# Kernel tuning notes

Measured on AMD Instinct MI355X. Metric: run time of the kernel, lower is better.

## Reference

```python
import jax, jax.numpy as jnp
import numpy as np

EPS = 1e-12
K_APPNP = 3
ALPHA = 0.5

def setup_inputs() -> dict:
    key = jax.random.key(0)
    kg, kz, k1, k2, k3 = jax.random.split(key, 5)
    N, out_dim, hid_dim = 10000, 128, 256
    g = jax.random.uniform(kg, (N, N), dtype=jnp.float32)
    z = jax.random.normal(kz, (N, out_dim), dtype=jnp.float32)
    def xavier(k, shape):
        fan_out, fan_in = shape
        lim = float(np.sqrt(6.0 / (fan_in + fan_out)))
        return jax.random.uniform(k, shape, jnp.float32, -lim, lim)
    # torch Linear weight is [out_features, in_features]
    W1 = xavier(k1, (hid_dim, out_dim))    # res1: out_dim -> hid_dim
    W1_ = xavier(k2, (hid_dim, hid_dim))   # res1_: hid -> hid
    W2 = xavier(k3, (out_dim, hid_dim))    # res2: hid -> out_dim
    return {"g": g, "z": z, "W1": W1, "W1_": W1_, "W2": W2}

def _graph_conv(g, x, W, act):
    # dropout is identity in eval mode
    return act((g @ x) @ W.T)

def _appnp(g, H):
    Z = H
    for _ in range(K_APPNP):
        Z = (1.0 - ALPHA) * (g @ Z) + ALPHA * H
    return Z

def reference(g, z, W1, W1_, W2):
    z1 = _graph_conv(g, z, W1, jax.nn.relu)       # [N, hid]
    z_ = _graph_conv(g, z1, W1_, jax.nn.relu)     # [N, hid]
    # torch.tensor(z_) detaches from the autograd graph
    zn = jax.lax.stop_gradient(z_)
    norm = jnp.maximum(jnp.linalg.norm(zn, axis=1, keepdims=True), EPS)
    zn = zn / norm                                 # F.normalize(p=2, dim=1)
    Z = _appnp(g, zn)                              # [N, hid]
    res = _graph_conv(g, z_, W2, jax.nn.sigmoid)   # [N, out]
    return (res, Z)
```

## Files before the change

### kernel.cpp

```cpp
#include <hip/hip_runtime.h>
#include <stdint.h>

typedef __attribute__((ext_vector_type(8))) short short8;
typedef __attribute__((ext_vector_type(4))) float f32x4;
typedef __attribute__((ext_vector_type(4))) unsigned short us4;

#define MFMA16(a,b,c) __builtin_amdgcn_mfma_f32_16x16x32_bf16((a),(b),(c),0,0,0)

static __device__ __forceinline__ float bf2f(unsigned short u){
  union { float f; unsigned int i; } c; c.i = ((unsigned int)u) << 16; return c.f;
}
static __device__ __forceinline__ unsigned short f2bf(float f){
  union { float f; unsigned int i; } c; c.f = f;
  unsigned int x = c.i;
  unsigned int r = x + 0x7fffu + ((x >> 16) & 1u);
  return (unsigned short)(r >> 16);
}
static __device__ __forceinline__ short8 pack8(const float* v){
  short8 r;
  #pragma unroll
  for (int i = 0; i < 8; ++i) r[i] = (short)f2bf(v[i]);
  return r;
}

typedef const __attribute__((address_space(1))) void cg_void;
typedef __attribute__((address_space(3))) void lds_void;
static __device__ __forceinline__ void gl_lds16(const void* g, void* l){
  __builtin_amdgcn_global_load_lds((cg_void*)g, (lds_void*)l, 16, 0, 0);
}

#define MROWS 10240LL
#define LDA   10048

__global__ void k_zero(unsigned short* __restrict__ g16, unsigned short* __restrict__ Tbuf){
  const long long i0 = (long long)blockIdx.x*256 + threadIdx.x;
  const long long NG = 192LL*LDA/8;
  short8 z = {0,0,0,0,0,0,0,0};
  for (long long c = i0; c < NG; c += (long long)gridDim.x*256)
    *(short8*)(g16 + 10048LL*LDA + c*8) = z;
  for (long long c = i0; c < 512*6; c += (long long)gridDim.x*256){
    int row = (int)(c/6), k = (int)(c%6);
    *(short8*)(Tbuf + (long long)row*LDA + 10000 + k*8) = z;
  }
}

__global__ void k_conv_w(const float* __restrict__ a, unsigned short* __restrict__ oa, int na4,
                         const float* __restrict__ b, unsigned short* __restrict__ ob, int nb4,
                         const float* __restrict__ c, unsigned short* __restrict__ oc, int nc4){
  for (int i = blockIdx.x*blockDim.x + threadIdx.x; i < na4 + nb4 + nc4;
       i += gridDim.x*blockDim.x){
    const float* src; unsigned short* dst; int j = i;
    if (j < na4){ src = a; dst = oa; }
    else if (j < na4 + nb4){ j -= na4; src = b; dst = ob; }
    else { j -= na4 + nb4; src = c; dst = oc; }
    float4 f = *(const float4*)(src + (long long)j*4);
    us4 v; v.x=f2bf(f.x); v.y=f2bf(f.y); v.z=f2bf(f.z); v.w=f2bf(f.w);
    *(us4*)(dst + (long long)j*4) = v;
  }
}

__global__ void k_tconv_z(const float* __restrict__ z, unsigned short* __restrict__ o){
  __shared__ unsigned short t[64][65];
  const int rb = blockIdx.x*64, cb = blockIdx.y*64;
  #pragma unroll
  for (int it = 0; it < 4; ++it){
    int idx = it*256 + threadIdx.x;
    int r = idx >> 4, c4 = (idx & 15) * 4;
    float4 f = {0.f,0.f,0.f,0.f};
    if (rb + r < 10000) f = *(const float4*)(z + (long long)(rb+r)*128 + cb + c4);
    t[c4+0][r] = f2bf(f.x); t[c4+1][r] = f2bf(f.y);
    t[c4+2][r] = f2bf(f.z); t[c4+3][r] = f2bf(f.w);
  }
  __syncthreads();
  #pragma unroll
  for (int it = 0; it < 4; ++it){
    int idx = it*256 + threadIdx.x;
    int ro = idx >> 4, co4 = (idx & 15) * 4;
    us4 v; v.x=t[ro][co4]; v.y=t[ro][co4+1]; v.z=t[ro][co4+2]; v.w=t[ro][co4+3];
    *(us4*)(o + (long long)(cb+ro)*LDA + rb + co4) = v;
  }
}

__global__ __launch_bounds__(256)
void k_gemm_t0(const float* __restrict__ g, const unsigned short* __restrict__ zT,
               unsigned short* __restrict__ g16, unsigned short* __restrict__ P, int S)
{
  constexpr int ldp = 128;
  __shared__ unsigned short sm[2][(64+128)*64];
  const int tid = threadIdx.x, w = tid >> 6, l = tid & 63;
  const int lr = l & 15, lk = l >> 4;
  const int wm = w >> 1, wn = w & 1;
  const int mBase = blockIdx.x * 64;
  const int s = blockIdx.z;
  const int kt0 = (157*s)/S, kt1 = (157*(s+1))/S;

  int arow[2], acol8[2];
  #pragma unroll
  for (int i = 0; i < 2; ++i){
    int ch = tid + 256*i;
    int row = ch >> 3, gr = ch & 7;
    arow[i] = row; acol8[i] = (gr ^ (row & 7)) * 8;
  }
  float fA[2][8];
  auto loadA = [&](int kt){
    #pragma unroll
    for (int i = 0; i < 2; ++i){
      int grow = mBase + arow[i];
      int col = kt*64 + acol8[i];
      if (grow < 10000 && col < 10000){
        float4 x = *(const float4*)(g + (long long)grow*10000 + col);
        float4 y = *(const float4*)(g + (long long)grow*10000 + col + 4);
        fA[i][0]=x.x; fA[i][1]=x.y; fA[i][2]=x.z; fA[i][3]=x.w;
        fA[i][4]=y.x; fA[i][5]=y.y; fA[i][6]=y.z; fA[i][7]=y.w;
      } else {
        #pragma unroll
        for (int j = 0; j < 8; ++j) fA[i][j] = 0.f;
      }
    }
  };
  auto writeA = [&](int buf, int kt){
    #pragma unroll
    for (int i = 0; i < 2; ++i){
      int ch = tid + 256*i;
      short8 v = pack8(fA[i]);
      *(short8*)(&sm[buf][ch*8]) = v;
      *(short8*)(g16 + (long long)(mBase + arow[i])*LDA + kt*64 + acol8[i]) = v;
    }
  };
  auto stageB = [&](int buf, int kt){
    unsigned short* dst = &sm[buf][64*64];
    const unsigned short* Bk = zT + (long long)kt*64;
    #pragma unroll
    for (int i = 0; i < 4; ++i){
      int c = i*256 + tid; int row = c >> 3, gr = c & 7;
      gl_lds16(Bk + (long long)row*LDA + ((gr ^ (row & 7))*8), dst + c*8);
    }
  };

  f32x4 acc[2][4];
  #pragma unroll
  for (int i = 0; i < 2; ++i)
    #pragma unroll
    for (int j = 0; j < 4; ++j){ f32x4 zz = {0.f,0.f,0.f,0.f}; acc[i][j] = zz; }

  loadA(kt0); stageB(0, kt0); writeA(0, kt0);
  int cur = 0;
  for (int kt = kt0; kt < kt1; ++kt){
    __syncthreads();
    const bool pf = (kt + 1 < kt1);
    if (pf){ loadA(kt+1); stageB(cur^1, kt+1); }
    const unsigned short* sp = &sm[cur][0];
    #pragma unroll
    for (int ks = 0; ks < 2; ++ks){
      short8 a[2], b[4];
      #pragma unroll
      for (int i = 0; i < 2; ++i){
        int row = wm*32 + i*16 + lr;
        a[i] = *(const short8*)(sp + row*64 + (((4*ks+lk) ^ (row & 7))*8));
      }
      #pragma unroll
      for (int j = 0; j < 4; ++j){
        int rb = wn*64 + j*16 + lr;
        b[j] = *(const short8*)(sp + 64*64 + rb*64 + (((4*ks+lk) ^ (rb & 7))*8));
      }
      #pragma unroll
      for (int i = 0; i < 2; ++i)
        #pragma unroll
        for (int j = 0; j < 4; ++j)
          acc[i][j] = MFMA16(a[i], b[j], acc[i][j]);
    }
    if (pf) writeA(cur^1, kt+1);
    cur ^= 1;
  }

  unsigned short* Pp = P + (long long)s*MROWS*ldp;
  #pragma unroll
  for (int i = 0; i < 2; ++i){
    const int row0 = mBase + wm*32 + i*16 + lk*4;
    #pragma unroll
    for (int j = 0; j < 4; ++j){
      const int col = wn*64 + j*16 + lr;
      #pragma unroll
      for (int r = 0; r < 4; ++r)
        Pp[(long long)(row0+r)*ldp + col] = f2bf(acc[i][j][r]);
    }
  }
}

__global__ __launch_bounds__(512)
void k_gemm8(const unsigned short* __restrict__ A,
             const unsigned short* __restrict__ B,
             unsigned short* __restrict__ P, int S, int ldp)
{
  __shared__ unsigned short sm[2][32768];

  const int tid = threadIdx.x;
  const int wid = tid >> 6, l = tid & 63;
  const int wm = wid >> 2, wn = wid & 3;
  const int lr = l & 15, lk = l >> 4;
  const int mBase = blockIdx.x * 256;
  const int nBase = blockIdx.y * 256;
  const int s = blockIdx.z;
  const int kt0 = (157*s)/S, kt1 = (157*(s+1))/S;

  const unsigned short* gsrc[8];
  int ldst[8];
  #pragma unroll
  for (int h = 0; h < 4; ++h){
    const unsigned short* base = (h < 2) ? A : B;
    const int rowBase = ((h < 2) ? mBase : nBase) + (h & 1) * 128;
    const int ldsOff = ((h < 2) ? 0 : 16384) + (h & 1) * 8192;
    #pragma unroll
    for (int i = 0; i < 2; ++i){
      int ch = tid + 512*i;
      int row = ch >> 3, gc = (ch & 7) ^ (row & 7);
      gsrc[h*2+i] = base + (long long)(rowBase + row)*LDA + gc*8;
      ldst[h*2+i] = ldsOff + ch*8;
    }
  }
  auto stage_tile = [&](unsigned short* dst, int kt){
    const long long ko = (long long)kt * 64;
    #pragma unroll
    for (int i = 0; i < 8; ++i)
      gl_lds16(gsrc[i] + ko, dst + ldst[i]);
  };

  f32x4 acc[8][4];
  #pragma unroll
  for (int i = 0; i < 8; ++i)
    #pragma unroll
    for (int j = 0; j < 4; ++j){ f32x4 zz = {0.f,0.f,0.f,0.f}; acc[i][j] = zz; }

  stage_tile(&sm[0][0], kt0);

  int cur = 0;
  for (int kt = kt0; kt < kt1; ++kt){
    const bool pf = (kt + 1 < kt1);
    unsigned short* nb = &sm[cur ^ 1][0];
    const unsigned short* sp = &sm[cur][0];

    if (pf){
      stage_tile(nb, kt + 1);
      __builtin_amdgcn_sched_barrier(0);
      asm volatile("s_waitcnt vmcnt(8)" ::: "memory");
    } else {
      asm volatile("s_waitcnt vmcnt(0)" ::: "memory");
    }
    __builtin_amdgcn_sched_barrier(0);
    __builtin_amdgcn_s_barrier();
    __builtin_amdgcn_sched_barrier(0);

    short8 bfr[4][2];
    #pragma unroll
    for (int jj = 0; jj < 4; ++jj){
      const int row = wn*64 + jj*16 + lr;
      #pragma unroll
      for (int ks = 0; ks < 2; ++ks)
        bfr[jj][ks] = *(const short8*)(sp + 16384 + row*64 + (((ks*4+lk) ^ (row & 7))*8));
    }
    #pragma unroll
    for (int ih = 0; ih < 2; ++ih){
      short8 af[4][2];
      #pragma unroll
      for (int ii = 0; ii < 4; ++ii){
        const int row = wm*128 + ih*64 + ii*16 + lr;
        #pragma unroll
        for (int ks = 0; ks < 2; ++ks)
          af[ii][ks] = *(const short8*)(sp + row*64 + (((ks*4+lk) ^ (row & 7))*8));
      }
      __builtin_amdgcn_s_setprio(1);
      #pragma unroll
      for (int ks = 0; ks < 2; ++ks)
        #pragma unroll
        for (int ii = 0; ii < 4; ++ii)
          #pragma unroll
          for (int jj = 0; jj < 4; ++jj)
            acc[ih*4+ii][jj] = MFMA16(af[ii][ks], bfr[jj][ks], acc[ih*4+ii][jj]);
      __builtin_amdgcn_s_setprio(0);
    }
    __builtin_amdgcn_sched_barrier(0);
    __builtin_amdgcn_s_barrier();
    __builtin_amdgcn_sched_barrier(0);
    cur ^= 1;
  }

  unsigned short* Pp = P + (long long)s*MROWS*ldp;
  #pragma unroll
  for (int i = 0; i < 8; ++i){
    const int row0 = mBase + wm*128 + i*16 + lk*4;
    #pragma unroll
    for (int j = 0; j < 4; ++j){
      const int col = nBase + wn*64 + j*16 + lr;
      #pragma unroll
      for (int r = 0; r < 4; ++r)
        Pp[(long long)(row0+r)*ldp + col] = f2bf(acc[i][j][r]);
    }
  }
}

template<int NW, int KW, int LDP, int S, int MODE>
__global__ __launch_bounds__(320)
void k_small(const unsigned short* __restrict__ P,
             const unsigned short* __restrict__ W,
             unsigned short* __restrict__ o1,
             unsigned short* __restrict__ o2,
             unsigned short* __restrict__ o3,
             float* __restrict__ of)
{
  const int tid = threadIdx.x, w = tid >> 6, l = tid & 63;
  const int lr = l & 15, lk = l >> 4;
  const int mBase = blockIdx.x * 80;
  constexpr int NF = NW/16;
  constexpr long long SSTR = MROWS*(long long)LDP;

  f32x4 acc[NF];
  #pragma unroll
  for (int f = 0; f < NF; ++f){ f32x4 zz = {0.f,0.f,0.f,0.f}; acc[f] = zz; }

  const unsigned short* ap = P + (long long)(mBase + 16*w + lr)*LDP + lk*8;
  #pragma unroll
  for (int kc = 0; kc < KW/32; ++kc){
    float av[8];
    short8 v0 = *(const short8*)(ap + kc*32);
    #pragma unroll
    for (int e = 0; e < 8; ++e) av[e] = bf2f((unsigned short)v0[e]);
    #pragma unroll
    for (int s2 = 1; s2 < S; ++s2){
      short8 v = *(const short8*)(ap + (long long)s2*SSTR + kc*32);
      #pragma unroll
      for (int e = 0; e < 8; ++e) av[e] += bf2f((unsigned short)v[e]);
    }
    short8 a = pack8(av);
    #pragma unroll
    for (int f = 0; f < NF; ++f){
      short8 b = *(const short8*)(W + (long long)(16*f+lr)*KW + kc*32 + lk*8);
      acc[f] = MFMA16(a, b, acc[f]);
    }
  }

  const int row0 = mBase + 16*w + lk*4;
  if constexpr (MODE == 2){
    #pragma unroll
    for (int f = 0; f < NF; ++f){
      const int col = 16*f + lr;
      #pragma unroll
      for (int r = 0; r < 4; ++r)
        of[(long long)(row0+r)*NW + col] = 1.0f / (1.0f + expf(-acc[f][r]));
    }
  } else if constexpr (MODE == 0){
    #pragma unroll
    for (int f = 0; f < NF; ++f){
      us4 v;
      #pragma unroll
      for (int r = 0; r < 4; ++r) v[r] = f2bf(fmaxf(acc[f][r], 0.0f));
      *(us4*)(o1 + (long long)(16*f+lr)*LDA + row0) = v;
    }
  } else {
    float ss[4] = {0.f,0.f,0.f,0.f};
    #pragma unroll
    for (int f = 0; f < NF; ++f)
      #pragma unroll
      for (int r = 0; r < 4; ++r){
        float v = fmaxf(acc[f][r], 0.0f);
        acc[f][r] = v;
        ss[r] += v*v;
      }
    #pragma unroll
    for (int r = 0; r < 4; ++r){
      #pragma unroll
      for (int off = 1; off <= 8; off <<= 1)
        ss[r] += __shfl_xor(ss[r], off, 64);
      ss[r] = 1.0f / fmaxf(sqrtf(ss[r]), 1e-12f);
    }
    #pragma unroll
    for (int f = 0; f < NF; ++f){
      const int col = 16*f + lr;
      us4 vz, vn;
      #pragma unroll
      for (int r = 0; r < 4; ++r){
        vz[r] = f2bf(acc[f][r]);
        vn[r] = f2bf(acc[f][r]*ss[r]);
        o3[(long long)(row0+r)*256 + col] = vn[r];
      }
      *(us4*)(o1 + (long long)col*LDA + row0) = vz;
      *(us4*)(o2 + (long long)col*LDA + row0) = vn;
    }
  }
}

__global__ void k_reduce_T(const unsigned short* __restrict__ P, int S, int ldp, int colOff,
                           unsigned short* __restrict__ outT,
                           const unsigned short* __restrict__ H)
{
  __shared__ unsigned short t[64][65];
  const int rb = blockIdx.x*64, cb = blockIdx.y*64;
  const long long stride = MROWS * (long long)ldp;
  #pragma unroll
  for (int it = 0; it < 4; ++it){
    int idx = it*256 + threadIdx.x;
    int r = idx >> 4, c4 = (idx & 15)*4;
    int row = rb + r;
    float sv[4] = {0.f,0.f,0.f,0.f};
    if (row < 10000){
      const unsigned short* p = P + (long long)row*ldp + colOff + cb + c4;
      for (int s2 = 0; s2 < S; ++s2){
        us4 tt = *(const us4*)(p + (long long)s2*stride);
        sv[0] += bf2f(tt.x); sv[1] += bf2f(tt.y);
        sv[2] += bf2f(tt.z); sv[3] += bf2f(tt.w);
      }
      us4 h = *(const us4*)(H + (long long)row*256 + cb + c4);
      sv[0] = 0.5f*sv[0] + 0.5f*bf2f(h.x);
      sv[1] = 0.5f*sv[1] + 0.5f*bf2f(h.y);
      sv[2] = 0.5f*sv[2] + 0.5f*bf2f(h.z);
      sv[3] = 0.5f*sv[3] + 0.5f*bf2f(h.w);
    }
    t[c4+0][r] = f2bf(sv[0]); t[c4+1][r] = f2bf(sv[1]);
    t[c4+2][r] = f2bf(sv[2]); t[c4+3][r] = f2bf(sv[3]);
  }
  __syncthreads();
  #pragma unroll
  for (int it = 0; it < 4; ++it){
    int idx = it*256 + threadIdx.x;
    int ro = idx >> 4, co4 = (idx & 15)*4;
    us4 v; v.x=t[ro][co4]; v.y=t[ro][co4+1]; v.z=t[ro][co4+2]; v.w=t[ro][co4+3];
    *(us4*)(outT + (long long)(cb+ro)*LDA + rb + co4) = v;
  }
}

__global__ void k_reduce2(const unsigned short* __restrict__ P, int S, int ldp,
                          float* __restrict__ out, const unsigned short* __restrict__ H)
{
  const long long stride = MROWS * (long long)ldp;
  const int idx = blockIdx.x*256 + threadIdx.x;
  const int row = idx >> 6;
  const int c4 = (idx & 63)*4;
  const unsigned short* p = P + (long long)row*ldp + c4;
  float sv[4] = {0.f,0.f,0.f,0.f};
  for (int s2 = 0; s2 < S; ++s2){
    us4 tt = *(const us4*)(p + (long long)s2*stride);
    sv[0] += bf2f(tt.x); sv[1] += bf2f(tt.y);
    sv[2] += bf2f(tt.z); sv[3] += bf2f(tt.w);
  }
  us4 h = *(const us4*)(H + (long long)row*256 + c4);
  float4 o;
  o.x = 0.5f*sv[0] + 0.5f*bf2f(h.x);
  o.y = 0.5f*sv[1] + 0.5f*bf2f(h.y);
  o.z = 0.5f*sv[2] + 0.5f*bf2f(h.z);
  o.w = 0.5f*sv[3] + 0.5f*bf2f(h.w);
  *(float4*)(out + (long long)row*256 + c4) = o;
}

extern "C" void kernel_launch(void* const* d_in, const int* in_sizes, int n_in,
                              void* d_out, int out_size, void* d_ws, size_t ws_size,
                              hipStream_t stream)
{
  const float* g   = (const float*)d_in[0];
  const float* z   = (const float*)d_in[1];
  const float* W1  = (const float*)d_in[2];
  const float* W1_ = (const float*)d_in[3];
  const float* W2  = (const float*)d_in[4];

  char* ws = (char*)d_ws;
  size_t off = 0;
  auto alloc = [&](size_t bytes)->void*{
    void* p = ws + off; off += (bytes + 255) & ~(size_t)255; return p;
  };
  unsigned short* g16  = (unsigned short*)alloc(10240ULL*10048*2);
  unsigned short* zT   = (unsigned short*)alloc(128ULL*10048*2);
  unsigned short* W1c  = (unsigned short*)alloc(256ULL*128*2);
  unsigned short* W1_c = (unsigned short*)alloc(256ULL*256*2);
  unsigned short* W2c  = (unsigned short*)alloc(128ULL*256*2);
  unsigned short* Tbuf = (unsigned short*)alloc(512ULL*10048*2);
  unsigned short* zn   = (unsigned short*)alloc(10000ULL*256*2);
  unsigned short* P    = (unsigned short*)alloc(10240ULL*1536*2);
  (void)ws_size; (void)in_sizes; (void)n_in; (void)out_size;

  float* res  = (float*)d_out;
  float* Zout = (float*)d_out + 10000LL*128;
  unsigned short* znT = Tbuf + 256LL*10048;

  k_zero<<<dim3(512), dim3(256), 0, stream>>>(g16, Tbuf);
  k_tconv_z<<<dim3(157,2), dim3(256), 0, stream>>>(z, zT);
  k_conv_w<<<dim3(120), dim3(256), 0, stream>>>(W1, W1c, 256*128/4,
                                                W1_, W1_c, 256*256/4,
                                                W2, W2c, 128*256/4);

  k_gemm_t0<<<dim3(157,1,3), dim3(256), 0, stream>>>(g, zT, g16, P, 3);
  k_small<256,128,128,3,0><<<dim3(125), dim3(320), 0, stream>>>(P, W1c, Tbuf, nullptr, nullptr, nullptr);
  k_gemm8<<<dim3(40,1,6), dim3(512), 0, stream>>>(g16, Tbuf, P, 6, 256);
  k_small<256,256,256,6,1><<<dim3(125), dim3(320), 0, stream>>>(P, W1_c, Tbuf, znT, zn, nullptr);
  k_gemm8<<<dim3(40,2,3), dim3(512), 0, stream>>>(g16, Tbuf, P, 3, 512);
  k_small<128,256,512,3,2><<<dim3(125), dim3(320), 0, stream>>>(P, W2c, nullptr, nullptr, nullptr, res);
  k_reduce_T<<<dim3(157,4), dim3(256), 0, stream>>>(P, 3, 512, 256, Tbuf, zn);
  k_gemm8<<<dim3(40,1,6), dim3(512), 0, stream>>>(g16, Tbuf, P, 6, 256);
  k_reduce_T<<<dim3(157,4), dim3(256), 0, stream>>>(P, 6, 256, 0, Tbuf, zn);
  k_gemm8<<<dim3(40,1,6), dim3(512), 0, stream>>>(g16, Tbuf, P, 6, 256);
  k_reduce2<<<dim3(2500), dim3(256), 0, stream>>>(P, 6, 256, Zout, zn);
}
```

Before: 558.7 us.

## Reassociate sigmoid branch to g@(z_W2ᵀ) and enlarge first GEMM tiles

The output branch is reassociated so that z_ is multiplied by W2ᵀ first, producing a 128-wide operand. The big graph GEMM for that branch then runs with N=128 through a new templated k_gemm8<BN>, followed by a dedicated sigmoid reduction. The fused 512-wide GEMM that handled both z_ and the normalized features is split into two passes over g16, trading some compute for an extra read of the large bf16 adjacency. The first fp32→bf16 GEMM moves to 256-row tiles with 512 threads and 6 K-splits, which also covers the padded rows, so the g16 pad zeroing is dropped.

Result: no change. 551.0 us (-1.4%).

```diff
diff --git a/kernel.cpp b/kernel.cpp
--- a/kernel.cpp
+++ b/kernel.cpp
@@ -32,14 +32,10 @@
 #define MROWS 10240LL
 #define LDA   10048
 
-__global__ void k_zero(unsigned short* __restrict__ g16, unsigned short* __restrict__ Tbuf){
-  const long long i0 = (long long)blockIdx.x*256 + threadIdx.x;
-  const long long NG = 192LL*LDA/8;
+__global__ void k_zero(unsigned short* __restrict__ Tbuf){
   short8 z = {0,0,0,0,0,0,0,0};
-  for (long long c = i0; c < NG; c += (long long)gridDim.x*256)
-    *(short8*)(g16 + 10048LL*LDA + c*8) = z;
-  for (long long c = i0; c < 512*6; c += (long long)gridDim.x*256){
-    int row = (int)(c/6), k = (int)(c%6);
+  for (int c = blockIdx.x*256 + threadIdx.x; c < 512*6; c += gridDim.x*256){
+    int row = c/6, k = c%6;
     *(short8*)(Tbuf + (long long)row*LDA + 10000 + k*8) = z;
   }
 }
@@ -81,30 +77,32 @@
   }
 }
 
-__global__ __launch_bounds__(256)
+__global__ __launch_bounds__(512)
 void k_gemm_t0(const float* __restrict__ g, const unsigned short* __restrict__ zT,
                unsigned short* __restrict__ g16, unsigned short* __restrict__ P, int S)
 {
   constexpr int ldp = 128;
-  __shared__ unsigned short sm[2][(64+128)*64];
-  const int tid = threadIdx.x, w = tid >> 6, l = tid & 63;
+  __shared__ unsigned short sm[2][24576];
+
+  const int tid = threadIdx.x;
+  const int wid = tid >> 6, l = tid & 63;
+  const int wm = wid >> 1, wn = wid & 1;
   const int lr = l & 15, lk = l >> 4;
-  const int wm = w >> 1, wn = w & 1;
-  const int mBase = blockIdx.x * 64;
+  const int mBase = blockIdx.x * 256;
   const int s = blockIdx.z;
   const int kt0 = (157*s)/S, kt1 = (157*(s+1))/S;
 
-  int arow[2], acol8[2];
-  #pragma unroll
-  for (int i = 0; i < 2; ++i){
-    int ch = tid + 256*i;
+  int arow[4], acol8[4];
+  #pragma unroll
+  for (int i = 0; i < 4; ++i){
+    int ch = tid + 512*i;
     int row = ch >> 3, gr = ch & 7;
-    arow[i] = row; acol8[i] = (gr ^ (row & 7)) * 8;
-  }
-  float fA[2][8];
+    arow[i] = row; acol8[i] = ((gr ^ (row & 7)) * 8);
+  }
+  float fA[4][8];
   auto loadA = [&](int kt){
     #pragma unroll
-    for (int i = 0; i < 2; ++i){
+    for (int i = 0; i < 4; ++i){
       int grow = mBase + arow[i];
       int col = kt*64 + acol8[i];
       if (grow < 10000 && col < 10000){
@@ -120,26 +118,26 @@
   };
   auto writeA = [&](int buf, int kt){
     #pragma unroll
-    for (int i = 0; i < 2; ++i){
-      int ch = tid + 256*i;
+    for (int i = 0; i < 4; ++i){
+      int ch = tid + 512*i;
       short8 v = pack8(fA[i]);
       *(short8*)(&sm[buf][ch*8]) = v;
       *(short8*)(g16 + (long long)(mBase + arow[i])*LDA + kt*64 + acol8[i]) = v;
     }
   };
   auto stageB = [&](int buf, int kt){
-    unsigned short* dst = &sm[buf][64*64];
+    unsigned short* dst = &sm[buf][16384];
     const unsigned short* Bk = zT + (long long)kt*64;
     #pragma unroll
-    for (int i = 0; i < 4; ++i){
-      int c = i*256 + tid; int row = c >> 3, gr = c & 7;
+    for (int i = 0; i < 2; ++i){
+      int c = i*512 + tid; int row = c >> 3, gr = c & 7;
       gl_lds16(Bk + (long long)row*LDA + ((gr ^ (row & 7))*8), dst + c*8);
     }
   };
 
-  f32x4 acc[2][4];
-  #pragma unroll
-  for (int i = 0; i < 2; ++i)
+  f32x4 acc[4][4];
+  #pragma unroll
+  for (int i = 0; i < 4; ++i)
     #pragma unroll
     for (int j = 0; j < 4; ++j){ f32x4 zz = {0.f,0.f,0.f,0.f}; acc[i][j] = zz; }
 
@@ -152,22 +150,20 @@
     const unsigned short* sp = &sm[cur][0];
     #pragma unroll
     for (int ks = 0; ks < 2; ++ks){
-      short8 a[2], b[4];
-      #pragma unroll
-      for (int i = 0; i < 2; ++i){
-        int row = wm*32 + i*16 + lr;
+      short8 a[4];
+      #pragma unroll
+      for (int i = 0; i < 4; ++i){
+        int row = wm*64 + i*16 + lr;
         a[i] = *(const short8*)(sp + row*64 + (((4*ks+lk) ^ (row & 7))*8));
       }
       #pragma unroll
       for (int j = 0; j < 4; ++j){
         int rb = wn*64 + j*16 + lr;
-        b[j] = *(const short8*)(sp + 64*64 + rb*64 + (((4*ks+lk) ^ (rb & 7))*8));
-      }
-      #pragma unroll
-      for (int i = 0; i < 2; ++i)
+        short8 b = *(const short8*)(sp + 16384 + rb*64 + (((4*ks+lk) ^ (rb & 7))*8));
         #pragma unroll
-        for (int j = 0; j < 4; ++j)
-          acc[i][j] = MFMA16(a[i], b[j], acc[i][j]);
+        for (int i = 0; i < 4; ++i)
+          acc[i][j] = MFMA16(a[i], b, acc[i][j]);
+      }
     }
     if (pf) writeA(cur^1, kt+1);
     cur ^= 1;
@@ -175,8 +171,8 @@
 
   unsigned short* Pp = P + (long long)s*MROWS*ldp;
   #pragma unroll
-  for (int i = 0; i < 2; ++i){
-    const int row0 = mBase + wm*32 + i*16 + lk*4;
+  for (int i = 0; i < 4; ++i){
+    const int row0 = mBase + wm*64 + i*16 + lk*4;
     #pragma unroll
     for (int j = 0; j < 4; ++j){
       const int col = wn*64 + j*16 + lr;
@@ -187,49 +183,54 @@
   }
 }
 
+template<int BN>
 __global__ __launch_bounds__(512)
 void k_gemm8(const unsigned short* __restrict__ A,
              const unsigned short* __restrict__ B,
-             unsigned short* __restrict__ P, int S, int ldp)
-{
-  __shared__ unsigned short sm[2][32768];
+             unsigned short* __restrict__ P, int S, int ldp, int nBase)
+{
+  constexpr int WNS = BN/4;
+  constexpr int NJ  = WNS/16;
+  constexpr int BCH = BN/64;
+  constexpr int NLD = 4 + BCH;
+  __shared__ unsigned short sm[2][16384 + BN*64];
 
   const int tid = threadIdx.x;
   const int wid = tid >> 6, l = tid & 63;
   const int wm = wid >> 2, wn = wid & 3;
   const int lr = l & 15, lk = l >> 4;
   const int mBase = blockIdx.x * 256;
-  const int nBase = blockIdx.y * 256;
   const int s = blockIdx.z;
   const int kt0 = (157*s)/S, kt1 = (157*(s+1))/S;
 
-  const unsigned short* gsrc[8];
-  int ldst[8];
-  #pragma unroll
-  for (int h = 0; h < 4; ++h){
-    const unsigned short* base = (h < 2) ? A : B;
-    const int rowBase = ((h < 2) ? mBase : nBase) + (h & 1) * 128;
-    const int ldsOff = ((h < 2) ? 0 : 16384) + (h & 1) * 8192;
-    #pragma unroll
-    for (int i = 0; i < 2; ++i){
-      int ch = tid + 512*i;
-      int row = ch >> 3, gc = (ch & 7) ^ (row & 7);
-      gsrc[h*2+i] = base + (long long)(rowBase + row)*LDA + gc*8;
-      ldst[h*2+i] = ldsOff + ch*8;
-    }
+  const unsigned short* gsrc[NLD];
+  int ldst[NLD];
+  #pragma unroll
+  for (int i = 0; i < 4; ++i){
+    int ch = tid + 512*i;
+    int row = ch >> 3, gc = (ch & 7) ^ (row & 7);
+    gsrc[i] = A + (long long)(mBase + row)*LDA + gc*8;
+    ldst[i] = ch*8;
+  }
+  #pragma unroll
+  for (int i = 0; i < BCH; ++i){
+    int ch = tid + 512*i;
+    int row = ch >> 3, gc = (ch & 7) ^ (row & 7);
+    gsrc[4+i] = B + (long long)(nBase + row)*LDA + gc*8;
+    ldst[4+i] = 16384 + ch*8;
   }
   auto stage_tile = [&](unsigned short* dst, int kt){
     const long long ko = (long long)kt * 64;
     #pragma unroll
-    for (int i = 0; i < 8; ++i)
+    for (int i = 0; i < NLD; ++i)
       gl_lds16(gsrc[i] + ko, dst + ldst[i]);
   };
 
-  f32x4 acc[8][4];
+  f32x4 acc[8][NJ];
   #pragma unroll
   for (int i = 0; i < 8; ++i)
     #pragma unroll
-    for (int j = 0; j < 4; ++j){ f32x4 zz = {0.f,0.f,0.f,0.f}; acc[i][j] = zz; }
+    for (int j = 0; j < NJ; ++j){ f32x4 zz = {0.f,0.f,0.f,0.f}; acc[i][j] = zz; }
 
   stage_tile(&sm[0][0], kt0);
 
@@ -242,7 +243,8 @@
     if (pf){
       stage_tile(nb, kt + 1);
       __builtin_amdgcn_sched_barrier(0);
-      asm volatile("s_waitcnt vmcnt(8)" ::: "memory");
+      if constexpr (BN == 256) asm volatile("s_waitcnt vmcnt(8)" ::: "memory");
+      else                     asm volatile("s_waitcnt vmcnt(6)" ::: "memory");
     } else {
       asm volatile("s_waitcnt vmcnt(0)" ::: "memory");
     }
@@ -250,10 +252,10 @@
     __builtin_amdgcn_s_barrier();
     __builtin_amdgcn_sched_barrier(0);
 
-    short8 bfr[4][2];
-    #pragma unroll
-    for (int jj = 0; jj < 4; ++jj){
-      const int row = wn*64 + jj*16 + lr;
+    short8 bfr[NJ][2];
+    #pragma unroll
+    for (int jj = 0; jj < NJ; ++jj){
+      const int row = wn*WNS + jj*16 + lr;
       #pragma unroll
       for (int ks = 0; ks < 2; ++ks)
         bfr[jj][ks] = *(const short8*)(sp + 16384 + row*64 + (((ks*4+lk) ^ (row & 7))*8));
@@ -274,7 +276,7 @@
         #pragma unroll
         for (int ii = 0; ii < 4; ++ii)
           #pragma unroll
-          for (int jj = 0; jj < 4; ++jj)
+          for (int jj = 0; jj < NJ; ++jj)
             acc[ih*4+ii][jj] = MFMA16(af[ii][ks], bfr[jj][ks], acc[ih*4+ii][jj]);
       __builtin_amdgcn_s_setprio(0);
     }
@@ -289,8 +291,8 @@
   for (int i = 0; i < 8; ++i){
     const int row0 = mBase + wm*128 + i*16 + lk*4;
     #pragma unroll
-    for (int j = 0; j < 4; ++j){
-      const int col = nBase + wn*64 + j*16 + lr;
+    for (int j = 0; j < NJ; ++j){
+      const int col = nBase + wn*WNS + j*16 + lr;
       #pragma unroll
       for (int r = 0; r < 4; ++r)
         Pp[(long long)(row0+r)*ldp + col] = f2bf(acc[i][j][r]);
@@ -305,7 +307,7 @@
              unsigned short* __restrict__ o1,
              unsigned short* __restrict__ o2,
              unsigned short* __restrict__ o3,
-             float* __restrict__ of)
+             int doRelu)
 {
   const int tid = threadIdx.x, w = tid >> 6, l = tid & 63;
   const int lr = l & 15, lk = l >> 4;
@@ -339,20 +341,16 @@
   }
 
   const int row0 = mBase + 16*w + lk*4;
-  if constexpr (MODE == 2){
-    #pragma unroll
-    for (int f = 0; f < NF; ++f){
-      const int col = 16*f + lr;
-      #pragma unroll
-      for (int r = 0; r < 4; ++r)
-        of[(long long)(row0+r)*NW + col] = 1.0f / (1.0f + expf(-acc[f][r]));
-    }
-  } else if constexpr (MODE == 0){
+  if constexpr (MODE == 0){
     #pragma unroll
     for (int f = 0; f < NF; ++f){
       us4 v;
       #pragma unroll
-      for (int r = 0; r < 4; ++r) v[r] = f2bf(fmaxf(acc[f][r], 0.0f));
+      for (int r = 0; r < 4; ++r){
+        float x = acc[f][r];
+        if (doRelu) x = fmaxf(x, 0.0f);
+        v[r] = f2bf(x);
+      }
       *(us4*)(o1 + (long long)(16*f+lr)*LDA + row0) = v;
     }
   } else {
@@ -375,15 +373,16 @@
     #pragma unroll
     for (int f = 0; f < NF; ++f){
       const int col = 16*f + lr;
-      us4 vz, vn;
+      us4 vn;
       #pragma unroll
       for (int r = 0; r < 4; ++r){
-        vz[r] = f2bf(acc[f][r]);
-        vn[r] = f2bf(acc[f][r]*ss[r]);
-        o3[(long long)(row0+r)*256 + col] = vn[r];
-      }
-      *(us4*)(o1 + (long long)col*LDA + row0) = vz;
-      *(us4*)(o2 + (long long)col*LDA + row0) = vn;
+        float zr = acc[f][r];
+        float nr = zr * ss[r];
+        vn[r] = f2bf(nr);
+        o2[(long long)(row0+r)*256 + col] = vn[r];
+        o3[(long long)(row0+r)*256 + col] = f2bf(zr);
+      }
+      *(us4*)(o1 + (long long)col*LDA + row0) = vn;
     }
   }
 }
@@ -425,6 +424,28 @@
     us4 v; v.x=t[ro][co4]; v.y=t[ro][co4+1]; v.z=t[ro][co4+2]; v.w=t[ro][co4+3];
     *(us4*)(outT + (long long)(cb+ro)*LDA + rb + co4) = v;
   }
+}
+
+__global__ void k_reduce_sig(const unsigned short* __restrict__ P, int S,
+                             float* __restrict__ out)
+{
+  const long long stride = MROWS * 128LL;
+  const int idx = blockIdx.x*256 + threadIdx.x;
+  const int row = idx >> 5;
+  const int c4 = (idx & 31)*4;
+  const unsigned short* p = P + (long long)row*128 + c4;
+  float sv[4] = {0.f,0.f,0.f,0.f};
+  for (int s2 = 0; s2 < S; ++s2){
+    us4 tt = *(const us4*)(p + (long long)s2*stride);
+    sv[0] += bf2f(tt.x); sv[1] += bf2f(tt.y);
+    sv[2] += bf2f(tt.z); sv[3] += bf2f(tt.w);
+  }
+  float4 o;
+  o.x = 1.0f/(1.0f + expf(-sv[0]));
+  o.y = 1.0f/(1.0f + expf(-sv[1]));
+  o.z = 1.0f/(1.0f + expf(-sv[2]));
+  o.w = 1.0f/(1.0f + expf(-sv[3]));
+  *(float4*)(out + (long long)row*128 + c4) = o;
 }
 
 __global__ void k_reduce2(const unsigned short* __restrict__ P, int S, int ldp,
@@ -472,28 +493,31 @@
   unsigned short* W2c  = (unsigned short*)alloc(128ULL*256*2);
   unsigned short* Tbuf = (unsigned short*)alloc(512ULL*10048*2);
   unsigned short* zn   = (unsigned short*)alloc(10000ULL*256*2);
+  unsigned short* Xbuf = (unsigned short*)alloc(10000ULL*256*2);
   unsigned short* P    = (unsigned short*)alloc(10240ULL*1536*2);
   (void)ws_size; (void)in_sizes; (void)n_in; (void)out_size;
 
   float* res  = (float*)d_out;
   float* Zout = (float*)d_out + 10000LL*128;
-  unsigned short* znT = Tbuf + 256LL*10048;
-
-  k_zero<<<dim3(512), dim3(256), 0, stream>>>(g16, Tbuf);
+  unsigned short* y2T = Tbuf + 256LL*LDA;
+
+  k_zero<<<dim3(12), dim3(256), 0, stream>>>(Tbuf);
   k_tconv_z<<<dim3(157,2), dim3(256), 0, stream>>>(z, zT);
   k_conv_w<<<dim3(120), dim3(256), 0, stream>>>(W1, W1c, 256*128/4,
                                                 W1_, W1_c, 256*256/4,
                                                 W2, W2c, 128*256/4);
 
-  k_gemm_t0<<<dim3(157,1,3), dim3(256), 0, stream>>>(g, zT, g16, P, 3);
-  k_small<256,128,128,3,0><<<dim3(125), dim3(320), 0, stream>>>(P, W1c, Tbuf, nullptr, nullptr, nullptr);
-  k_gemm8<<<dim3(40,1,6), dim3(512), 0, stream>>>(g16, Tbuf, P, 6, 256);
-  k_small<256,256,256,6,1><<<dim3(125), dim3(320), 0, stream>>>(P, W1_c, Tbuf, znT, zn, nullptr);
-  k_gemm8<<<dim3(40,2,3), dim3(512), 0, stream>>>(g16, Tbuf, P, 3, 512);
-  k_small<128,256,512,3,2><<<dim3(125), dim3(320), 0, stream>>>(P, W2c, nullptr, nullptr, nullptr, res);
-  k_reduce_T<<<dim3(157,4), dim3(256), 0, stream>>>(P, 3, 512, 256, Tbuf, zn);
-  k_gemm8<<<dim3(40,1,6), dim3(512), 0, stream>>>(g16, Tbuf, P, 6, 256);
+  k_gemm_t0<<<dim3(40,1,6), dim3(512), 0, stream>>>(g, zT, g16, P, 6);
+  k_small<256,128,128,6,0><<<dim3(125), dim3(320), 0, stream>>>(P, W1c, Tbuf, nullptr, nullptr, 1);
+  k_gemm8<256><<<dim3(40,1,6), dim3(512), 0, stream>>>(g16, Tbuf, P, 6, 256, 0);
+  k_small<256,256,256,6,1><<<dim3(125), dim3(320), 0, stream>>>(P, W1_c, Tbuf, zn, Xbuf, 0);
+  k_small<128,256,256,1,0><<<dim3(125), dim3(320), 0, stream>>>(Xbuf, W2c, y2T, nullptr, nullptr, 0);
+  k_gemm8<256><<<dim3(40,1,6), dim3(512), 0, stream>>>(g16, Tbuf, P, 6, 256, 0);
   k_reduce_T<<<dim3(157,4), dim3(256), 0, stream>>>(P, 6, 256, 0, Tbuf, zn);
-  k_gemm8<<<dim3(40,1,6), dim3(512), 0, stream>>>(g16, Tbuf, P, 6, 256);
+  k_gemm8<128><<<dim3(40,1,6), dim3(512), 0, stream>>>(g16, y2T, P, 6, 128, 0);
+  k_reduce_sig<<<dim3(1250), dim3(256), 0, stream>>>(P, 6, res);
+  k_gemm8<256><<<dim3(40,1,6), dim3(512), 0, stream>>>(g16, Tbuf, P, 6, 256, 0);
+  k_reduce_T<<<dim3(157,4), dim3(256), 0, stream>>>(P, 6, 256, 0, Tbuf, zn);
+  k_gemm8<256><<<dim3(40,1,6), dim3(512), 0, stream>>>(g16, Tbuf, P, 6, 256, 0);
   k_reduce2<<<dim3(2500), dim3(256), 0, stream>>>(P, 6, 256, Zout, zn);
 }
```
